# Optimization experiments

Measured on AMD Instinct MI355X. Metric: run time of the kernel, lower is better.

Reference implementation:

```python
import jax, jax.numpy as jnp
import numpy as np

B, S, N = 1, 256, 384
MSA_S, Z_D = 64, 128
H, C_H = 8, 32
C_OPM = 32
INF = 1e9

def ln(x, w, b):
    mu = jnp.mean(x, -1, keepdims=True)
    var = jnp.mean(jnp.square(x - mu), -1, keepdims=True)
    return (x - mu) * jax.lax.rsqrt(var + 1e-5) * w + b

def setup_inputs() -> dict:
    key = jax.random.key(0)
    ks = jax.random.split(key, 16)
    def lin(k, out_d, in_d):
        return jax.random.normal(k, (out_d, in_d), jnp.float32) / np.sqrt(in_d)
    return {
        "z": jax.random.normal(ks[0], (B, N, N, Z_D), jnp.float32),
        "m": jax.random.normal(ks[1], (B, S, N, MSA_S), jnp.float32),
        "token_mask": jnp.ones((B, N, N), jnp.float32),
        "msa_mask": jnp.ones((B, S, N), jnp.float32),
        "norm_z_w": jnp.ones((Z_D,), jnp.float32), "norm_z_b": jnp.zeros((Z_D,), jnp.float32),
        "proj_z_w": lin(ks[2], H, Z_D),
        "norm_m_w": jnp.ones((MSA_S,), jnp.float32), "norm_m_b": jnp.zeros((MSA_S,), jnp.float32),
        "proj_m_w": lin(ks[3], H * C_H, MSA_S),
        "proj_g_w": lin(ks[4], H * C_H, MSA_S),
        "pwa_proj_o_w": lin(ks[5], MSA_S, H * C_H),
        "trans_norm_w": jnp.ones((MSA_S,), jnp.float32), "trans_norm_b": jnp.zeros((MSA_S,), jnp.float32),
        "fc1_w": lin(ks[6], 4 * MSA_S, MSA_S),
        "fc2_w": lin(ks[7], 4 * MSA_S, MSA_S),
        "fc3_w": lin(ks[8], MSA_S, 4 * MSA_S),
        "opm_norm_w": jnp.ones((MSA_S,), jnp.float32), "opm_norm_b": jnp.zeros((MSA_S,), jnp.float32),
        "proj_a_w": lin(ks[9], C_OPM, MSA_S),
        "proj_b_w": lin(ks[10], C_OPM, MSA_S),
        "opm_proj_o_w": lin(ks[11], Z_D, C_OPM * C_OPM),
        "opm_proj_o_b": jnp.zeros((Z_D,), jnp.float32),
    }

def reference(z, m, token_mask, msa_mask,
              norm_z_w, norm_z_b, proj_z_w,
              norm_m_w, norm_m_b, proj_m_w, proj_g_w, pwa_proj_o_w,
              trans_norm_w, trans_norm_b, fc1_w, fc2_w, fc3_w,
              opm_norm_w, opm_norm_b, proj_a_w, proj_b_w, opm_proj_o_w, opm_proj_o_b):
    # --- PairWeightedAveraging: pair-biased, gated MSA row attention ---
    b_full = ln(z, norm_z_w, norm_z_b) @ proj_z_w.T                     # [B,N,N,H]
    bias = jnp.transpose(b_full, (0, 3, 1, 2)) + (1.0 - token_mask[:, None]) * (-INF)
    w = jax.nn.softmax(bias, axis=-1)                                   # [B,H,N,N]
    mn = ln(m, norm_m_w, norm_m_b)
    v = (mn @ proj_m_w.T).reshape(B, S, N, H, C_H)                      # [B,S,N,H,c]
    g = jax.nn.sigmoid(mn @ proj_g_w.T)                                 # [B,S,N,H*c]
    o = jnp.einsum('bhij,bsjhd->bsihd', w, v).reshape(B, S, N, H * C_H)
    m = m + (g * o) @ pwa_proj_o_w.T
    # --- MSA transition (SwiGLU) ---
    tn = ln(m, trans_norm_w, trans_norm_b)
    m = m + (jax.nn.silu(tn @ fc1_w.T) * (tn @ fc2_w.T)) @ fc3_w.T
    # --- OuterProductMean -> pair update ---
    mk = msa_mask[..., None]                                            # [B,S,N,1]
    on = ln(m, opm_norm_w, opm_norm_b)
    a = (on @ proj_a_w.T) * mk                                          # [B,S,N,c]
    bb = (on @ proj_b_w.T) * mk                                         # [B,S,N,c]
    num_mask = jnp.clip(jnp.einsum('bsi,bsj->bij', msa_mask, msa_mask), 1.0, None)[..., None]
    opm = jnp.einsum('bsic,bsjd->bijcd', a, bb).reshape(B, N, N, C_OPM * C_OPM) / num_mask
    z = z + opm @ opm_proj_o_w.T + opm_proj_o_b
    return (z, m)
```

## Files before the change

kernel.cpp:

```cpp
#include <hip/hip_runtime.h>
#include <math.h>

constexpr int NRES = 384;
constexpr int NSEQ = 256;
constexpr int DM   = 64;
constexpr int DZ   = 128;
constexpr int NH   = 8;
constexpr int DH   = 32;
constexpr int HC   = NH * DH;
constexpr int DOP  = 32;
constexpr int FF   = 4 * DM;

constexpr int NPAIR = NRES * NRES;
constexpr int NROWS = NSEQ * NRES;
constexpr int ZTOT  = NPAIR * DZ;
constexpr int SD    = NSEQ * DH;

typedef unsigned short ushort_t;
typedef unsigned char uchar_t;
typedef long long i64;
typedef __attribute__((ext_vector_type(8))) short short8;
typedef __attribute__((ext_vector_type(4))) float f32x4;
typedef __attribute__((ext_vector_type(4))) int int4_t;

__device__ __forceinline__ float wred_sum(float v) {
    #pragma unroll
    for (int off = 32; off; off >>= 1) v += __shfl_xor(v, off, 64);
    return v;
}
__device__ __forceinline__ float sigm(float x) { return 1.0f / (1.0f + expf(-x)); }
__device__ __forceinline__ ushort_t cvt_bf(float f) {
    unsigned u = __float_as_uint(f);
    unsigned r = (u + 0x7FFFu + ((u >> 16) & 1u)) >> 16;
    return (ushort_t)r;
}
__device__ __forceinline__ float cvt_f(ushort_t h) {
    return __uint_as_float(((unsigned)h) << 16);
}
__device__ __forceinline__ uchar_t cvt_f8(float f) {
    return (uchar_t)(__builtin_amdgcn_cvt_pk_fp8_f32(f, 0.0f, 0, 0) & 0xff);
}
__device__ __forceinline__ f32x4 mfma16(short8 a, short8 b, f32x4 c) {
    return __builtin_amdgcn_mfma_f32_16x16x32_bf16(a, b, c, 0, 0, 0);
}
__device__ __forceinline__ f32x4 mfma16f8(i64 a, i64 b, f32x4 c) {
    return __builtin_amdgcn_mfma_f32_16x16x32_fp8_fp8(a, b, c, 0, 0, 0);
}
__device__ __forceinline__ void gld16(const void* g, void* l) {
    __builtin_amdgcn_global_load_lds(
        (const __attribute__((address_space(1))) unsigned int*)g,
        (__attribute__((address_space(3))) unsigned int*)l, 16, 0, 0);
}

__global__ __launch_bounds__(256) void k_prep(const float* __restrict__ f1,
                                              const float* __restrict__ f2,
                                              const float* __restrict__ f3,
                                              const float* __restrict__ opW,
                                              const float* __restrict__ pmw,
                                              const float* __restrict__ pgw,
                                              const float* __restrict__ pow_,
                                              const float* __restrict__ paw,
                                              const float* __restrict__ pbw,
                                              const float* __restrict__ pzw,
                                              ushort_t* __restrict__ f1b,
                                              ushort_t* __restrict__ f2b,
                                              ushort_t* __restrict__ f3b,
                                              uchar_t* __restrict__ opW8,
                                              ushort_t* __restrict__ pmwb,
                                              ushort_t* __restrict__ pgwb,
                                              ushort_t* __restrict__ powb,
                                              ushort_t* __restrict__ abwb,
                                              ushort_t* __restrict__ pzwb) {
    int i = blockIdx.x * 256 + threadIdx.x;
    opW8[i] = cvt_f8(opW[i]);
    if (i < FF * DM) {
        f1b[i] = cvt_bf(f1[i]);
        f2b[i] = cvt_bf(f2[i]);
        f3b[i] = cvt_bf(f3[i]);
    }
    if (i < HC * DM) {
        pmwb[i] = cvt_bf(pmw[i]);
        pgwb[i] = cvt_bf(pgw[i]);
        powb[i] = cvt_bf(pow_[i]);
    }
    if (i < 2 * DOP * DM) {
        abwb[i] = cvt_bf(i < DOP * DM ? paw[i] : pbw[i - DOP * DM]);
    }
    if (i < 16 * DZ) {
        pzwb[i] = (i < NH * DZ) ? cvt_bf(pzw[i]) : (ushort_t)0;
    }
}

__global__ __launch_bounds__(256) void k_biassm(const float* __restrict__ z,
                                                const float* __restrict__ nzw,
                                                const float* __restrict__ nzb,
                                                const ushort_t* __restrict__ pzwb,
                                                const float* __restrict__ tmask,
                                                ushort_t* __restrict__ wsb) {
    int i = blockIdx.x;
    __shared__ ushort_t Azl[128][136];
    __shared__ ushort_t Bl[16][136];
    __shared__ float ob[8][388];
    __shared__ float wln[128], bln[128];
    int t = threadIdx.x;
    if (t < 128) { wln[t] = nzw[t]; bln[t] = nzb[t]; }
    int wave = t >> 6, lane = t & 63;
    int lk = (lane >> 4) * 8, lr = lane & 15;
    int wr = wave * 32;
    for (int idx = t * 8; idx < 16 * DZ; idx += 256 * 8) {
        int row = idx >> 7, col = idx & 127;
        *(short8*)&Bl[row][col] = *(const short8*)&pzwb[idx];
    }
    __syncthreads();
    for (int c = 0; c < 3; c++) {
        {
            int jl = t >> 1, cb = (t & 1) * 64;
            const float* src = &z[((size_t)i * NRES + c * 128 + jl) * DZ + cb];
            float4 v[16];
            float s1 = 0.0f, s2 = 0.0f;
            #pragma unroll
            for (int q = 0; q < 16; q++) {
                v[q] = *(const float4*)&src[q * 4];
                s1 += v[q].x + v[q].y + v[q].z + v[q].w;
                s2 += v[q].x * v[q].x + v[q].y * v[q].y + v[q].z * v[q].z + v[q].w * v[q].w;
            }
            s1 += __shfl_xor(s1, 1, 64);
            s2 += __shfl_xor(s2, 1, 64);
            float mu = s1 * (1.0f / 128.0f);
            float var = s2 * (1.0f / 128.0f) - mu * mu;
            float rs = rsqrtf(var + 1e-5f);
            #pragma unroll
            for (int q = 0; q < 8; q++) {
                float4 xa = v[2 * q], xb = v[2 * q + 1];
                int base = cb + q * 8;
                short8 o;
                o[0] = (short)cvt_bf((xa.x - mu) * rs * wln[base + 0] + bln[base + 0]);
                o[1] = (short)cvt_bf((xa.y - mu) * rs * wln[base + 1] + bln[base + 1]);
                o[2] = (short)cvt_bf((xa.z - mu) * rs * wln[base + 2] + bln[base + 2]);
                o[3] = (short)cvt_bf((xa.w - mu) * rs * wln[base + 3] + bln[base + 3]);
                o[4] = (short)cvt_bf((xb.x - mu) * rs * wln[base + 4] + bln[base + 4]);
                o[5] = (short)cvt_bf((xb.y - mu) * rs * wln[base + 5] + bln[base + 5]);
                o[6] = (short)cvt_bf((xb.z - mu) * rs * wln[base + 6] + bln[base + 6]);
                o[7] = (short)cvt_bf((xb.w - mu) * rs * wln[base + 7] + bln[base + 7]);
                *(short8*)&Azl[jl][base] = o;
            }
        }
        __syncthreads();
        f32x4 acc[2] = {};
        #pragma unroll
        for (int ks = 0; ks < 4; ks++) {
            short8 b = *(const short8*)&Bl[lr][ks * 32 + lk];
            short8 a0 = *(const short8*)&Azl[wr + lr][ks * 32 + lk];
            short8 a1 = *(const short8*)&Azl[wr + 16 + lr][ks * 32 + lk];
            acc[0] = mfma16(a0, b, acc[0]);
            acc[1] = mfma16(a1, b, acc[1]);
        }
        if (lr < NH) {
            #pragma unroll
            for (int ri = 0; ri < 2; ri++) {
                int jb = c * 128 + wr + 16 * ri + (lane >> 4) * 4;
                #pragma unroll
                for (int r = 0; r < 4; r++)
                    ob[lr][jb + r] = acc[ri][r];
            }
        }
        __syncthreads();
    }
    int h = wave * 2 + (lane >> 5);
    int l32 = lane & 31;
    int jb = l32 * 12;
    const float* tm = &tmask[(size_t)i * NRES];
    float vals[12];
    float mx = -1e30f;
    #pragma unroll
    for (int q = 0; q < 12; q++) {
        float v = ob[h][jb + q] + (1.0f - tm[jb + q]) * (-1e9f);
        vals[q] = v;
        mx = fmaxf(mx, v);
    }
    #pragma unroll
    for (int off = 16; off; off >>= 1) mx = fmaxf(mx, __shfl_xor(mx, off, 64));
    float sum = 0.0f;
    #pragma unroll
    for (int q = 0; q < 12; q++) { vals[q] = expf(vals[q] - mx); sum += vals[q]; }
    #pragma unroll
    for (int off = 16; off; off >>= 1) sum += __shfl_xor(sum, off, 64);
    float inv = 1.0f / sum;
    ushort_t* o = &wsb[(size_t)h * NPAIR + (size_t)i * NRES + jb];
    #pragma unroll
    for (int q = 0; q < 12; q++) o[q] = cvt_bf(vals[q] * inv);
}

__global__ __launch_bounds__(256) void k_ln64(const float* __restrict__ src,
                                              const float* __restrict__ lw,
                                              const float* __restrict__ lb,
                                              ushort_t* __restrict__ dst) {
    int wave = threadIdx.x >> 6, lane = threadIdx.x & 63;
    int r = blockIdx.x * 4 + wave;
    float x = src[(size_t)r * DM + lane];
    float mu = wred_sum(x) * (1.0f / 64.0f);
    float d = x - mu;
    float var = wred_sum(d * d) * (1.0f / 64.0f);
    dst[(size_t)r * DM + lane] = cvt_bf(d * rsqrtf(var + 1e-5f) * lw[lane] + lb[lane]);
}

__global__ __launch_bounds__(256) void k_vproj_mfma(const ushort_t* __restrict__ A,
                                                    const ushort_t* __restrict__ Bt,
                                                    ushort_t* __restrict__ vtt) {
    int m0 = blockIdx.y * 64, n0c = blockIdx.x * 64;
    __shared__ ushort_t Al[64][40];
    __shared__ ushort_t Bl[64][40];
    __shared__ ushort_t ot[64][72];
    int t = threadIdx.x;
    int srow = t >> 2, sko = (t & 3) * 8;
    int wave = t >> 6, lane = t & 63;
    int wr = (wave >> 1) * 32, wc = (wave & 1) * 32;
    int lk = (lane >> 4) * 8, lr = lane & 15;
    f32x4 acc[2][2] = {};
    for (int k0 = 0; k0 < DM; k0 += 32) {
        *(short8*)&Al[srow][sko] = *(const short8*)&A[(size_t)(m0 + srow) * DM + k0 + sko];
        *(short8*)&Bl[srow][sko] = *(const short8*)&Bt[(size_t)(n0c + srow) * DM + k0 + sko];
        __syncthreads();
        short8 a0 = *(const short8*)&Al[wr + lr][lk];
        short8 a1 = *(const short8*)&Al[wr + 16 + lr][lk];
        short8 b0 = *(const short8*)&Bl[wc + lr][lk];
        short8 b1 = *(const short8*)&Bl[wc + 16 + lr][lk];
        acc[0][0] = mfma16(a0, b0, acc[0][0]);
        acc[0][1] = mfma16(a0, b1, acc[0][1]);
        acc[1][0] = mfma16(a1, b0, acc[1][0]);
        acc[1][1] = mfma16(a1, b1, acc[1][1]);
        __syncthreads();
    }
    #pragma unroll
    for (int ri = 0; ri < 2; ri++)
        #pragma unroll
        for (int ci = 0; ci < 2; ci++) {
            int rowb = wr + 16 * ri + (lane >> 4) * 4;
            int colb = wc + 16 * ci + lr;
            #pragma unroll
            for (int r = 0; r < 4; r++)
                ot[colb][rowb + r] = cvt_bf(acc[ri][ci][r]);
        }
    __syncthreads();
    int s = m0 / NRES, n0 = m0 % NRES;
    int h0 = n0c >> 5;
    int orow = t >> 2, seg = (t & 3) * 16;
    short8 v0 = *(const short8*)&ot[orow][seg];
    short8 v1 = *(const short8*)&ot[orow][seg + 8];
    int hh = orow >> 5, dd = orow & 31;
    ushort_t* dst = &vtt[(((size_t)(h0 + hh) * SD) + s * DH + dd) * NRES + n0 + seg];
    *(short8*)&dst[0] = v0;
    *(short8*)&dst[8] = v1;
}

__global__ __launch_bounds__(256) void k_tr(const ushort_t* __restrict__ src,
                                            ushort_t* __restrict__ dst,
                                            int R, int C) {
    size_t bs = (size_t)R * C;
    const ushort_t* s = src + blockIdx.z * bs;
    ushort_t* d = dst + blockIdx.z * bs;
    int r0 = blockIdx.y * 64, c0 = blockIdx.x * 64;
    __shared__ ushort_t tile[64][72];
    int t = threadIdx.x;
    int tr = t >> 2, tc = (t & 3) * 16;
    *(short8*)&tile[tr][tc]     = *(const short8*)&s[(size_t)(r0 + tr) * C + c0 + tc];
    *(short8*)&tile[tr][tc + 8] = *(const short8*)&s[(size_t)(r0 + tr) * C + c0 + tc + 8];
    __syncthreads();
    short8 o0, o1;
    #pragma unroll
    for (int i = 0; i < 8; i++) {
        o0[i] = (short)tile[tc + i][tr];
        o1[i] = (short)tile[tc + 8 + i][tr];
    }
    *(short8*)&d[(size_t)(c0 + tr) * R + r0 + tc]     = o0;
    *(short8*)&d[(size_t)(c0 + tr) * R + r0 + tc + 8] = o1;
}

__global__ __launch_bounds__(256) void k_attn_mfma(const ushort_t* __restrict__ wsb,
                                                   const ushort_t* __restrict__ vtt,
                                                   ushort_t* __restrict__ otb2) {
    int h = blockIdx.z;
    const ushort_t* A  = wsb + (size_t)h * NPAIR;
    const ushort_t* Bt = vtt + (size_t)h * SD * NRES;
    int m0 = blockIdx.y * 128, n0 = blockIdx.x * 128;
    __shared__ ushort_t Al[128 * 32];
    __shared__ ushort_t Bl[128 * 32];
    int t = threadIdx.x;
    int w = t >> 6, lane = t & 63;
    int wr = (w >> 1) * 64, wc = (w & 1) * 64;
    int lq = lane >> 4, lr = lane & 15;
    int rS = w * 16 + (lane >> 2);
    int cqs = (((lane & 3) ^ ((rS >> 1) & 3)) << 3);
    f32x4 acc[4][4] = {};
    for (int k0 = 0; k0 < NRES; k0 += 32) {
        gld16(&A [(size_t)(m0 + rS)      * NRES + k0 + cqs], &Al[(w * 16) * 32]);
        gld16(&A [(size_t)(m0 + 64 + rS) * NRES + k0 + cqs], &Al[(64 + w * 16) * 32]);
        gld16(&Bt[(size_t)(n0 + rS)      * NRES + k0 + cqs], &Bl[(w * 16) * 32]);
        gld16(&Bt[(size_t)(n0 + 64 + rS) * NRES + k0 + cqs], &Bl[(64 + w * 16) * 32]);
        __syncthreads();
        short8 af[4], bf2[4];
        #pragma unroll
        for (int i = 0; i < 4; i++) {
            int ra = wr + 16 * i + lr;
            int rb = wc + 16 * i + lr;
            af[i]  = *(const short8*)&Al[ra * 32 + ((lq ^ ((ra >> 1) & 3)) << 3)];
            bf2[i] = *(const short8*)&Bl[rb * 32 + ((lq ^ ((rb >> 1) & 3)) << 3)];
        }
        #pragma unroll
        for (int ri = 0; ri < 4; ri++)
            #pragma unroll
            for (int ci = 0; ci < 4; ci++)
                acc[ri][ci] = mfma16(af[ri], bf2[ci], acc[ri][ci]);
        __syncthreads();
    }
    #pragma unroll
    for (int ri = 0; ri < 4; ri++)
        #pragma unroll
        for (int ci = 0; ci < 4; ci++) {
            int row0 = m0 + wr + 16 * ri + (lane >> 4) * 4;
            int col  = n0 + wc + 16 * ci + lr;
            int s = col >> 5, dd = col & 31;
            #pragma unroll
            for (int r = 0; r < 4; r++)
                otb2[((size_t)s * NRES + row0 + r) * HC + h * DH + dd] = cvt_bf(acc[ri][ci][r]);
        }
}

__global__ __launch_bounds__(256) void k_gateout(const ushort_t* __restrict__ A,
                                                 const ushort_t* __restrict__ Bg,
                                                 const ushort_t* __restrict__ otb2,
                                                 const ushort_t* __restrict__ Bo,
                                                 const float* __restrict__ m,
                                                 float* __restrict__ mout,
                                                 const float* __restrict__ tnw,
                                                 const float* __restrict__ tnb,
                                                 ushort_t* __restrict__ tn_bf) {
    int m0 = blockIdx.x * 64;
    __shared__ ushort_t Al[64][72];
    __shared__ ushort_t Bl[64][72];
    __shared__ ushort_t go[64][264];
    int t = threadIdx.x;
    int srow = t >> 2, sko = (t & 3) * 16;
    int wave = t >> 6, lane = t & 63;
    int wr = (wave >> 1) * 32, wc = (wave & 1) * 32;
    int lk = (lane >> 4) * 8, lr = lane & 15;
    float tw = tnw[lane], tb = tnb[lane];
    {
        const ushort_t* arow = &A[(size_t)(m0 + srow) * DM + sko];
        *(short8*)&Al[srow][sko]     = *(const short8*)&arow[0];
        *(short8*)&Al[srow][sko + 8] = *(const short8*)&arow[8];
    }
    __syncthreads();
    short8 a[2][2];
    a[0][0] = *(const short8*)&Al[wr + lr][lk];
    a[0][1] = *(const short8*)&Al[wr + lr][32 + lk];
    a[1][0] = *(const short8*)&Al[wr + 16 + lr][lk];
    a[1][1] = *(const short8*)&Al[wr + 16 + lr][32 + lk];
    for (int nq = 0; nq < 4; nq++) {
        __syncthreads();
        {
            const ushort_t* brow = &Bg[(size_t)(nq * 64 + srow) * DM + sko];
            *(short8*)&Bl[srow][sko]     = *(const short8*)&brow[0];
            *(short8*)&Bl[srow][sko + 8] = *(const short8*)&brow[8];
        }
        __syncthreads();
        f32x4 acc[2][2] = {};
        #pragma unroll
        for (int ks = 0; ks < 2; ks++) {
            short8 b0 = *(const short8*)&Bl[wc + lr][ks * 32 + lk];
            short8 b1 = *(const short8*)&Bl[wc + 16 + lr][ks * 32 + lk];
            acc[0][0] = mfma16(a[0][ks], b0, acc[0][0]);
            acc[0][1] = mfma16(a[0][ks], b1, acc[0][1]);
            acc[1][0] = mfma16(a[1][ks], b0, acc[1][0]);
            acc[1][1] = mfma16(a[1][ks], b1, acc[1][1]);
        }
        #pragma unroll
        for (int ri = 0; ri < 2; ri++)
            #pragma unroll
            for (int ci = 0; ci < 2; ci++) {
                int lrow = wr + 16 * ri + (lane >> 4) * 4;
                int col  = nq * 64 + wc + 16 * ci + lr;
                #pragma unroll
                for (int r = 0; r < 4; r++) {
                    float ov = cvt_f(otb2[(size_t)(m0 + lrow + r) * HC + col]);
                    go[lrow + r][col] = cvt_bf(sigm(acc[ri][ci][r]) * ov);
                }
            }
    }
    f32x4 acc[2][2] = {};
    for (int k0 = 0; k0 < HC; k0 += 32) {
        __syncthreads();
        *(short8*)&Bl[t >> 2][(t & 3) * 8] = *(const short8*)&Bo[(size_t)(t >> 2) * HC + k0 + (t & 3) * 8];
        __syncthreads();
        short8 a0 = *(const short8*)&go[wr + lr][k0 + lk];
        short8 a1 = *(const short8*)&go[wr + 16 + lr][k0 + lk];
        short8 b0 = *(const short8*)&Bl[wc + lr][lk];
        short8 b1 = *(const short8*)&Bl[wc + 16 + lr][lk];
        acc[0][0] = mfma16(a0, b0, acc[0][0]);
        acc[0][1] = mfma16(a0, b1, acc[0][1]);
        acc[1][0] = mfma16(a1, b0, acc[1][0]);
        acc[1][1] = mfma16(a1, b1, acc[1][1]);
    }
    __syncthreads();
    #pragma unroll
    for (int ri = 0; ri < 2; ri++)
        #pragma unroll
        for (int ci = 0; ci < 2; ci++) {
            int lrow0 = wr + 16 * ri + (lane >> 4) * 4;
            int col   = wc + 16 * ci + lr;
            #pragma unroll
            for (int r = 0; r < 4; r++) {
                size_t idx = (size_t)(m0 + lrow0 + r) * DM + col;
                float v = m[idx] + acc[ri][ci][r];
                mout[idx] = v;
                go[lrow0 + r][col] = cvt_bf(v);
            }
        }
    __syncthreads();
    for (int rr = 0; rr < 16; rr++) {
        int row = wave * 16 + rr;
        float x = cvt_f(go[row][lane]);
        float mu = wred_sum(x) * (1.0f / 64.0f);
        float d = x - mu;
        float var = wred_sum(d * d) * (1.0f / 64.0f);
        tn_bf[(size_t)(m0 + row) * DM + lane] = cvt_bf(d * rsqrtf(var + 1e-5f) * tw + tb);
    }
}

__global__ __launch_bounds__(256) void k_fctrans(const ushort_t* __restrict__ A,
                                                 const ushort_t* __restrict__ B1,
                                                 const ushort_t* __restrict__ B2,
                                                 const ushort_t* __restrict__ B3,
                                                 float* __restrict__ mio,
                                                 const float* __restrict__ onw,
                                                 const float* __restrict__ onb,
                                                 ushort_t* __restrict__ onb_bf) {
    int m0 = blockIdx.x * 64;
    __shared__ ushort_t Al[64][72];
    __shared__ ushort_t B1l[64][72];
    __shared__ ushort_t B2l[64][72];
    __shared__ ushort_t hhl[64][264];
    int t = threadIdx.x;
    int srow = t >> 2, sko = (t & 3) * 16;
    int wave = t >> 6, lane = t & 63;
    int wr = (wave >> 1) * 32, wc = (wave & 1) * 32;
    int lk = (lane >> 4) * 8, lr = lane & 15;
    float ow = onw[lane], ob = onb[lane];
    {
        const ushort_t* arow = &A[(size_t)(m0 + srow) * DM + sko];
        *(short8*)&Al[srow][sko]     = *(const short8*)&arow[0];
        *(short8*)&Al[srow][sko + 8] = *(const short8*)&arow[8];
    }
    __syncthreads();
    short8 a[2][2];
    a[0][0] = *(const short8*)&Al[wr + lr][lk];
    a[0][1] = *(const short8*)&Al[wr + lr][32 + lk];
    a[1][0] = *(const short8*)&Al[wr + 16 + lr][lk];
    a[1][1] = *(const short8*)&Al[wr + 16 + lr][32 + lk];
    for (int nq = 0; nq < 4; nq++) {
        __syncthreads();
        {
            const ushort_t* b1r = &B1[(size_t)(nq * 64 + srow) * DM + sko];
            const ushort_t* b2r = &B2[(size_t)(nq * 64 + srow) * DM + sko];
            *(short8*)&B1l[srow][sko]     = *(const short8*)&b1r[0];
            *(short8*)&B1l[srow][sko + 8] = *(const short8*)&b1r[8];
            *(short8*)&B2l[srow][sko]     = *(const short8*)&b2r[0];
            *(short8*)&B2l[srow][sko + 8] = *(const short8*)&b2r[8];
        }
        __syncthreads();
        f32x4 acc1[2][2] = {}, acc2[2][2] = {};
        #pragma unroll
        for (int ks = 0; ks < 2; ks++) {
            short8 p0 = *(const short8*)&B1l[wc + lr][ks * 32 + lk];
            short8 p1 = *(const short8*)&B1l[wc + 16 + lr][ks * 32 + lk];
            short8 q0 = *(const short8*)&B2l[wc + lr][ks * 32 + lk];
            short8 q1 = *(const short8*)&B2l[wc + 16 + lr][ks * 32 + lk];
            acc1[0][0] = mfma16(a[0][ks], p0, acc1[0][0]);
            acc1[0][1] = mfma16(a[0][ks], p1, acc1[0][1]);
            acc1[1][0] = mfma16(a[1][ks], p0, acc1[1][0]);
            acc1[1][1] = mfma16(a[1][ks], p1, acc1[1][1]);
            acc2[0][0] = mfma16(a[0][ks], q0, acc2[0][0]);
            acc2[0][1] = mfma16(a[0][ks], q1, acc2[0][1]);
            acc2[1][0] = mfma16(a[1][ks], q0, acc2[1][0]);
            acc2[1][1] = mfma16(a[1][ks], q1, acc2[1][1]);
        }
        #pragma unroll
        for (int ri = 0; ri < 2; ri++)
            #pragma unroll
            for (int ci = 0; ci < 2; ci++) {
                int lrow = wr + 16 * ri + (lane >> 4) * 4;
                int col  = nq * 64 + wc + 16 * ci + lr;
                #pragma unroll
                for (int r = 0; r < 4; r++) {
                    float a1v = acc1[ri][ci][r], a2v = acc2[ri][ci][r];
                    hhl[lrow + r][col] = cvt_bf(a1v * sigm(a1v) * a2v);
                }
            }
    }
    f32x4 acc[2][2] = {};
    for (int k0 = 0; k0 < FF; k0 += 32) {
        __syncthreads();
        *(short8*)&B1l[t >> 2][(t & 3) * 8] = *(const short8*)&B3[(size_t)(t >> 2) * FF + k0 + (t & 3) * 8];
        __syncthreads();
        short8 a0 = *(const short8*)&hhl[wr + lr][k0 + lk];
        short8 a1 = *(const short8*)&hhl[wr + 16 + lr][k0 + lk];
        short8 b0 = *(const short8*)&B1l[wc + lr][lk];
        short8 b1 = *(const short8*)&B1l[wc + 16 + lr][lk];
        acc[0][0] = mfma16(a0, b0, acc[0][0]);
        acc[0][1] = mfma16(a0, b1, acc[0][1]);
        acc[1][0] = mfma16(a1, b0, acc[1][0]);
        acc[1][1] = mfma16(a1, b1, acc[1][1]);
    }
    __syncthreads();
    #pragma unroll
    for (int ri = 0; ri < 2; ri++)
        #pragma unroll
        for (int ci = 0; ci < 2; ci++) {
            int lrow0 = wr + 16 * ri + (lane >> 4) * 4;
            int col   = wc + 16 * ci + lr;
            #pragma unroll
            for (int r = 0; r < 4; r++) {
                size_t idx = (size_t)(m0 + lrow0 + r) * DM + col;
                float v = mio[idx] + acc[ri][ci][r];
                mio[idx] = v;
                hhl[lrow0 + r][col] = cvt_bf(v);
            }
        }
    __syncthreads();
    for (int rr = 0; rr < 16; rr++) {
        int row = wave * 16 + rr;
        float x = cvt_f(hhl[row][lane]);
        float mu = wred_sum(x) * (1.0f / 64.0f);
        float d = x - mu;
        float var = wred_sum(d * d) * (1.0f / 64.0f);
        onb_bf[(size_t)(m0 + row) * DM + lane] = cvt_bf(d * rsqrtf(var + 1e-5f) * ow + ob);
    }
}

__global__ __launch_bounds__(256) void k_ab_mfma(const ushort_t* __restrict__ A,
                                                 const ushort_t* __restrict__ Bt,
                                                 const float* __restrict__ smask,
                                                 ushort_t* __restrict__ abuf,
                                                 ushort_t* __restrict__ bbuf) {
    int m0 = blockIdx.x * 64;
    __shared__ ushort_t Al[64][40];
    __shared__ ushort_t Bl[64][40];
    int t = threadIdx.x;
    int srow = t >> 2, sko = (t & 3) * 8;
    int wave = t >> 6, lane = t & 63;
    int wr = (wave >> 1) * 32, wc = (wave & 1) * 32;
    int lk = (lane >> 4) * 8, lr = lane & 15;
    f32x4 acc[2][2] = {};
    for (int k0 = 0; k0 < DM; k0 += 32) {
        *(short8*)&Al[srow][sko] = *(const short8*)&A[(size_t)(m0 + srow) * DM + k0 + sko];
        *(short8*)&Bl[srow][sko] = *(const short8*)&Bt[(size_t)srow * DM + k0 + sko];
        __syncthreads();
        short8 a0 = *(const short8*)&Al[wr + lr][lk];
        short8 a1 = *(const short8*)&Al[wr + 16 + lr][lk];
        short8 b0 = *(const short8*)&Bl[wc + lr][lk];
        short8 b1 = *(const short8*)&Bl[wc + 16 + lr][lk];
        acc[0][0] = mfma16(a0, b0, acc[0][0]);
        acc[0][1] = mfma16(a0, b1, acc[0][1]);
        acc[1][0] = mfma16(a1, b0, acc[1][0]);
        acc[1][1] = mfma16(a1, b1, acc[1][1]);
        __syncthreads();
    }
    #pragma unroll
    for (int ri = 0; ri < 2; ri++)
        #pragma unroll
        for (int ci = 0; ci < 2; ci++) {
            int row0 = m0 + wr + 16 * ri + (lane >> 4) * 4;
            int col  = wc + 16 * ci + lr;
            #pragma unroll
            for (int r = 0; r < 4; r++) {
                int rr = row0 + r;
                int s = rr / NRES, n = rr % NRES;
                float v = acc[ri][ci][r] * smask[rr];
                if (col < DOP)
                    abuf[(size_t)s * (NRES * DOP) + n * DOP + col] = cvt_bf(v);
                else
                    bbuf[(size_t)s * (NRES * DOP) + n * DOP + (col - DOP)] = cvt_bf(v);
            }
        }
}

__global__ __launch_bounds__(256) void k_msum(const float* __restrict__ smask,
                                              float* __restrict__ msum) {
    int i0 = blockIdx.y * 64, j0 = blockIdx.x * 64;
    __shared__ float As[16][64];
    __shared__ float Bs[16][64];
    int t = threadIdx.x;
    int ty = t >> 4, tx = t & 15;
    float acc[4][4] = {};
    for (int k0 = 0; k0 < NSEQ; k0 += 16) {
        int kk = t >> 4, x4 = (t & 15) * 4;
        *(float4*)&As[kk][x4] = *(const float4*)&smask[(size_t)(k0 + kk) * NRES + i0 + x4];
        *(float4*)&Bs[kk][x4] = *(const float4*)&smask[(size_t)(k0 + kk) * NRES + j0 + x4];
        __syncthreads();
        #pragma unroll
        for (int k = 0; k < 16; k++) {
            float4 a4 = *(const float4*)&As[k][ty * 4];
            float4 b4 = *(const float4*)&Bs[k][tx * 4];
            float ar[4] = {a4.x, a4.y, a4.z, a4.w};
            float br[4] = {b4.x, b4.y, b4.z, b4.w};
            #pragma unroll
            for (int i2 = 0; i2 < 4; i2++)
                #pragma unroll
                for (int j2 = 0; j2 < 4; j2++)
                    acc[i2][j2] += ar[i2] * br[j2];
        }
        __syncthreads();
    }
    #pragma unroll
    for (int r = 0; r < 4; r++) {
        float4 o4 = make_float4(fmaxf(acc[r][0], 1.0f), fmaxf(acc[r][1], 1.0f),
                                fmaxf(acc[r][2], 1.0f), fmaxf(acc[r][3], 1.0f));
        *(float4*)&msum[(size_t)(i0 + ty * 4 + r) * NRES + j0 + tx * 4] = o4;
    }
}

__global__ __launch_bounds__(256) void k_opm_mfma(const ushort_t* __restrict__ At,
                                                  const ushort_t* __restrict__ Bt,
                                                  uchar_t* __restrict__ opmc8) {
    int m0 = blockIdx.y * 128;
    int n0 = blockIdx.x * 128;
    __shared__ ushort_t Al[128 * 64];
    __shared__ ushort_t Bl[128 * 64];
    __shared__ uchar_t ol[16 * 1040];
    int t = threadIdx.x;
    int w = t >> 6, lane = t & 63;
    int wr = (w >> 1) * 64, wc = (w & 1) * 64;
    int lq = lane >> 4, lr = lane & 15;
    int rS = lane >> 3;
    int cqs = (((lane & 7) ^ rS) << 3);
    f32x4 acc[4][4] = {};
    for (int k0 = 0; k0 < NSEQ; k0 += 64) {
        #pragma unroll
        for (int g = 0; g < 4; g++) {
            int row = w * 32 + g * 8;
            gld16(&At[(size_t)(m0 + row + rS) * NSEQ + k0 + cqs], &Al[row * 64]);
            gld16(&Bt[(size_t)(n0 + row + rS) * NSEQ + k0 + cqs], &Bl[row * 64]);
        }
        __syncthreads();
        #pragma unroll
        for (int kk = 0; kk < 2; kk++) {
            short8 af[4], bf2[4];
            #pragma unroll
            for (int i = 0; i < 4; i++) {
                int ra = wr + 16 * i + lr;
                int rb = wc + 16 * i + lr;
                af[i]  = *(const short8*)&Al[ra * 64 + (((kk * 4 + lq) ^ (ra & 7)) << 3)];
                bf2[i] = *(const short8*)&Bl[rb * 64 + (((kk * 4 + lq) ^ (rb & 7)) << 3)];
            }
            #pragma unroll
            for (int ri = 0; ri < 4; ri++)
                #pragma unroll
                for (int ci = 0; ci < 4; ci++)
                    acc[ri][ci] = mfma16(bf2[ci], af[ri], acc[ri][ci]);
        }
        __syncthreads();
    }
    #pragma unroll
    for (int ri = 0; ri < 4; ri++)
        #pragma unroll
        for (int ci = 0; ci < 4; ci++) {
            int ml = wr + 16 * ri + lr;
            int il = ml >> 5, c = ml & 31;
            int nl = wc + 16 * ci + lq * 4;
            int j = nl >> 5, dd = nl & 31;
            int p = il * 4 + j;
            int p01  = __builtin_amdgcn_cvt_pk_fp8_f32(acc[ri][ci][0], acc[ri][ci][1], 0, 0);
            int pall = __builtin_amdgcn_cvt_pk_fp8_f32(acc[ri][ci][2], acc[ri][ci][3], p01, 1);
            *(int*)&ol[p * 1040 + (c << 5) + dd] = pall;
        }
    __syncthreads();
    {
        int p = t >> 4, off = (t & 15) * 64;
        int ilg = (m0 >> 5) + (p >> 2);
        int jg  = (n0 >> 5) + (p & 3);
        uchar_t* dst = &opmc8[((size_t)(ilg * NRES + jg) << 10) + off];
        const uchar_t* src = &ol[p * 1040 + off];
        #pragma unroll
        for (int q = 0; q < 4; q++)
            *(int4_t*)&dst[q * 16] = *(const int4_t*)&src[q * 16];
    }
}

__global__ __launch_bounds__(256) void k_proj_mfma(const uchar_t* __restrict__ A,
                                                   const uchar_t* __restrict__ Bt,
                                                   const float* __restrict__ opB,
                                                   const float* __restrict__ msum,
                                                   const float* __restrict__ zin,
                                                   float* __restrict__ zout,
                                                   int ib) {
    int m0 = blockIdx.x * 128;
    __shared__ uchar_t Al[128 * 32];
    __shared__ uchar_t Bl[128 * 32];
    int t = threadIdx.x;
    int w = t >> 6, lane = t & 63;
    int wr = (w >> 1) * 64, wc = (w & 1) * 64;
    int lq = lane >> 4, lr = lane & 15;
    int rS = lane >> 1, cS = (lane & 1) * 16;
    f32x4 acc[4][4] = {};
    for (int k0 = 0; k0 < 1024; k0 += 32) {
        gld16(&A [(size_t)(m0 + w * 32 + rS) * 1024 + k0 + cS], &Al[(w * 32) * 32]);
        gld16(&Bt[(size_t)(w * 32 + rS)      * 1024 + k0 + cS], &Bl[(w * 32) * 32]);
        __syncthreads();
        i64 af[4], bf2[4];
        #pragma unroll
        for (int i = 0; i < 4; i++) {
            af[i]  = *(const i64*)&Al[(wr + 16 * i + lr) * 32 + lq * 8];
            bf2[i] = *(const i64*)&Bl[(wc + 16 * i + lr) * 32 + lq * 8];
        }
        #pragma unroll
        for (int ri = 0; ri < 4; ri++)
            #pragma unroll
            for (int ci = 0; ci < 4; ci++)
                acc[ri][ci] = mfma16f8(bf2[ci], af[ri], acc[ri][ci]);
        __syncthreads();
    }
    #pragma unroll
    for (int ri = 0; ri < 4; ri++) {
        int p = m0 + wr + 16 * ri + lr;
        size_t G = (size_t)ib * NRES + p;
        float inv = 1.0f / msum[G];
        #pragma unroll
        for (int ci = 0; ci < 4; ci++) {
            int e0 = wc + 16 * ci + lq * 4;
            float4 zv = *(const float4*)&zin[G * DZ + e0];
            float4 bv = *(const float4*)&opB[e0];
            float4 o4;
            o4.x = zv.x + acc[ri][ci][0] * inv + bv.x;
            o4.y = zv.y + acc[ri][ci][1] * inv + bv.y;
            o4.z = zv.z + acc[ri][ci][2] * inv + bv.z;
            o4.w = zv.w + acc[ri][ci][3] * inv + bv.w;
            *(float4*)&zout[G * DZ + e0] = o4;
        }
    }
}

extern "C" void kernel_launch(void* const* d_in, const int* in_sizes, int n_in,
                              void* d_out, int out_size, void* d_ws, size_t ws_size,
                              hipStream_t stream) {
    const float* z     = (const float*)d_in[0];
    const float* m     = (const float*)d_in[1];
    const float* tmask = (const float*)d_in[2];
    const float* smask = (const float*)d_in[3];
    const float* nzw   = (const float*)d_in[4];
    const float* nzb   = (const float*)d_in[5];
    const float* pzw   = (const float*)d_in[6];
    const float* nmw   = (const float*)d_in[7];
    const float* nmb   = (const float*)d_in[8];
    const float* pmw   = (const float*)d_in[9];
    const float* pgw   = (const float*)d_in[10];
    const float* pow_  = (const float*)d_in[11];
    const float* tnw   = (const float*)d_in[12];
    const float* tnb_  = (const float*)d_in[13];
    const float* f1    = (const float*)d_in[14];
    const float* f2    = (const float*)d_in[15];
    const float* f3    = (const float*)d_in[16];
    const float* onw   = (const float*)d_in[17];
    const float* onb   = (const float*)d_in[18];
    const float* paw   = (const float*)d_in[19];
    const float* pbw   = (const float*)d_in[20];
    const float* opW   = (const float*)d_in[21];
    const float* opB   = (const float*)d_in[22];

    float* zout = (float*)d_out;
    float* mout = zout + ZTOT;

    char* W = (char*)d_ws;
    ushort_t* wsb  = (ushort_t*)(W + 4718592);
    ushort_t* mnb  = (ushort_t*)(W + 7077888);
    ushort_t* vtt  = (ushort_t*)(W + 69992448);
    ushort_t* otb2 = (ushort_t*)(W + 120324096);
    ushort_t* tn_bf  = vtt;
    ushort_t* onb_bf = mnb;
    ushort_t* abuf = (ushort_t*)(W + 69992448 + 12582912);
    ushort_t* bbuf = (ushort_t*)(W + 69992448 + 18874368);

    bool big = ws_size >= 348200000ull;
    int ichunk, nchunks;
    uchar_t *opmc8, *opW8;
    ushort_t *abt, *bbt;
    float* msum;
    ushort_t *f1b, *f2b, *f3b, *pmwb, *pgwb, *powb, *abwb, *pzwb;
    if (big) {
        ichunk = NRES; nchunks = 1;
        opmc8 = (uchar_t*)(W + 19660800);
        abt  = (ushort_t*)(W + 321650688);
        bbt  = (ushort_t*)(W + 327942144);
        msum = (float*)(W + 346816512);
        f1b  = (ushort_t*)(W + 347406336);
        f2b  = (ushort_t*)(W + 347439104);
        f3b  = (ushort_t*)(W + 347471872);
        opW8 = (uchar_t*)(W + 347504640);
        pmwb = (ushort_t*)(W + 347766784);
        pgwb = (ushort_t*)(W + 347799552);
        powb = (ushort_t*)(W + 347832320);
        abwb = (ushort_t*)(W + 347865088);
        pzwb = (ushort_t*)(W + 347873280);
    } else {
        ichunk = 96; nchunks = 4;
        opmc8 = (uchar_t*)(W + 19660800);
        abt  = otb2;
        bbt  = (ushort_t*)(W + 120324096 + 6291456);
        msum = (float*)(W + 170655744);
        f1b  = (ushort_t*)(W + 171245568);
        f2b  = (ushort_t*)(W + 171278336);
        f3b  = (ushort_t*)(W + 171311104);
        opW8 = (uchar_t*)(W + 171343872);
        pmwb = (ushort_t*)(W + 171606016);
        pgwb = (ushort_t*)(W + 171638784);
        powb = (ushort_t*)(W + 171671552);
        abwb = (ushort_t*)(W + 171704320);
        pzwb = (ushort_t*)(W + 171712512);
    }

    k_prep<<<512, 256, 0, stream>>>(f1, f2, f3, opW, pmw, pgw, pow_, paw, pbw, pzw,
                                    f1b, f2b, f3b, opW8, pmwb, pgwb, powb, abwb, pzwb);

    k_biassm<<<NRES, 256, 0, stream>>>(z, nzw, nzb, pzwb, tmask, wsb);
    k_ln64<<<NROWS / 4, 256, 0, stream>>>(m, nmw, nmb, mnb);
    k_vproj_mfma<<<dim3(HC / 64, NROWS / 64), 256, 0, stream>>>(mnb, pmwb, vtt);
    k_attn_mfma<<<dim3(SD / 128, NRES / 128, NH), 256, 0, stream>>>(wsb, vtt, otb2);
    k_gateout<<<NROWS / 64, 256, 0, stream>>>(mnb, pgwb, otb2, powb, m, mout, tnw, tnb_, tn_bf);

    k_fctrans<<<NROWS / 64, 256, 0, stream>>>(tn_bf, f1b, f2b, f3b, mout, onw, onb, onb_bf);

    k_ab_mfma<<<NROWS / 64, 256, 0, stream>>>(onb_bf, abwb, smask, abuf, bbuf);
    k_tr<<<dim3((NRES * DOP) / 64, NSEQ / 64, 2), 256, 0, stream>>>(abuf, abt, NSEQ, NRES * DOP);
    k_msum<<<dim3(NRES / 64, NRES / 64), 256, 0, stream>>>(smask, msum);
    for (int cb = 0; cb < nchunks; cb++) {
        int ib = cb * ichunk;
        const ushort_t* Achunk = abt + (size_t)(ib * DOP) * NSEQ;
        k_opm_mfma<<<dim3((NRES * DOP) / 128, (ichunk * DOP) / 128), 256, 0, stream>>>(Achunk, bbt, opmc8);
        k_proj_mfma<<<(ichunk * NRES) / 128, 256, 0, stream>>>(opmc8, opW8, opB, msum, z, zout, ib);
    }
}
```

Measured before the change: 454.4 us.

## Fuse OPM output projection into outer-product kernel, dropping fp8 intermediate

The outer-product kernel now projects its 16 pair tiles (each 32x32 fp8) through the 1024x128 output weight itself, using fp8 MFMA with weights staged through LDS, and writes the final z update directly. This removes the separate projection kernel and the global round trip of the large fp8 opm intermediate. In exchange, every block re-reads the full projection weight and the projection runs with only 16 rows per MFMA tile in each block, so efficiency is lower. LDS is reused between the A/B staging and the output tile.

```diff
diff --git a/kernel.cpp b/kernel.cpp
--- a/kernel.cpp
+++ b/kernel.cpp
@@ -621,18 +621,26 @@
 
 __global__ __launch_bounds__(256) void k_opm_mfma(const ushort_t* __restrict__ At,
                                                   const ushort_t* __restrict__ Bt,
-                                                  uchar_t* __restrict__ opmc8) {
+                                                  const uchar_t* __restrict__ opW8,
+                                                  const float* __restrict__ opB,
+                                                  const float* __restrict__ msum,
+                                                  const float* __restrict__ zin,
+                                                  float* __restrict__ zout,
+                                                  int ib) {
     int m0 = blockIdx.y * 128;
     int n0 = blockIdx.x * 128;
-    __shared__ ushort_t Al[128 * 64];
-    __shared__ ushort_t Bl[128 * 64];
-    __shared__ uchar_t ol[16 * 1040];
+    __shared__ ushort_t ABl[2 * 128 * 64];
+    __shared__ uchar_t Wl[128 * 128];
+    ushort_t* Al = ABl;
+    ushort_t* Bl = ABl + 128 * 64;
+    uchar_t* ol = (uchar_t*)ABl;
     int t = threadIdx.x;
     int w = t >> 6, lane = t & 63;
     int wr = (w >> 1) * 64, wc = (w & 1) * 64;
     int lq = lane >> 4, lr = lane & 15;
     int rS = lane >> 3;
     int cqs = (((lane & 7) ^ rS) << 3);
+    int cS8 = (((lane & 7) ^ rS) << 4);
     f32x4 acc[4][4] = {};
     for (int k0 = 0; k0 < NSEQ; k0 += 64) {
         #pragma unroll
@@ -674,66 +682,44 @@
             *(int*)&ol[p * 1040 + (c << 5) + dd] = pall;
         }
     __syncthreads();
+    f32x4 accp[2] = {};
+    for (int kc = 0; kc < 8; kc++) {
+        #pragma unroll
+        for (int g = 0; g < 4; g++) {
+            int row = w * 32 + g * 8;
+            gld16(&opW8[(size_t)(row + rS) * 1024 + kc * 128 + cS8], &Wl[row * 128]);
+        }
+        __syncthreads();
+        #pragma unroll
+        for (int ls = 0; ls < 4; ls++) {
+            i64 af = *(const i64*)&ol[lr * 1040 + kc * 128 + ls * 32 + lq * 8];
+            int l = ls * 2 + (lq >> 1);
+            int wo = (lq & 1) * 8;
+            #pragma unroll
+            for (int et = 0; et < 2; et++) {
+                int er = w * 32 + et * 16 + lr;
+                i64 bf = *(const i64*)&Wl[er * 128 + ((l ^ (er & 7)) << 4) + wo];
+                accp[et] = mfma16f8(bf, af, accp[et]);
+            }
+        }
+        __syncthreads();
+    }
     {
-        int p = t >> 4, off = (t & 15) * 64;
-        int ilg = (m0 >> 5) + (p >> 2);
+        int p = lr;
+        int ilg = ib + (m0 >> 5) + (p >> 2);
         int jg  = (n0 >> 5) + (p & 3);
-        uchar_t* dst = &opmc8[((size_t)(ilg * NRES + jg) << 10) + off];
-        const uchar_t* src = &ol[p * 1040 + off];
-        #pragma unroll
-        for (int q = 0; q < 4; q++)
-            *(int4_t*)&dst[q * 16] = *(const int4_t*)&src[q * 16];
-    }
-}
-
-__global__ __launch_bounds__(256) void k_proj_mfma(const uchar_t* __restrict__ A,
-                                                   const uchar_t* __restrict__ Bt,
-                                                   const float* __restrict__ opB,
-                                                   const float* __restrict__ msum,
-                                                   const float* __restrict__ zin,
-                                                   float* __restrict__ zout,
-                                                   int ib) {
-    int m0 = blockIdx.x * 128;
-    __shared__ uchar_t Al[128 * 32];
-    __shared__ uchar_t Bl[128 * 32];
-    int t = threadIdx.x;
-    int w = t >> 6, lane = t & 63;
-    int wr = (w >> 1) * 64, wc = (w & 1) * 64;
-    int lq = lane >> 4, lr = lane & 15;
-    int rS = lane >> 1, cS = (lane & 1) * 16;
-    f32x4 acc[4][4] = {};
-    for (int k0 = 0; k0 < 1024; k0 += 32) {
-        gld16(&A [(size_t)(m0 + w * 32 + rS) * 1024 + k0 + cS], &Al[(w * 32) * 32]);
-        gld16(&Bt[(size_t)(w * 32 + rS)      * 1024 + k0 + cS], &Bl[(w * 32) * 32]);
-        __syncthreads();
-        i64 af[4], bf2[4];
-        #pragma unroll
-        for (int i = 0; i < 4; i++) {
-            af[i]  = *(const i64*)&Al[(wr + 16 * i + lr) * 32 + lq * 8];
-            bf2[i] = *(const i64*)&Bl[(wc + 16 * i + lr) * 32 + lq * 8];
-        }
-        #pragma unroll
-        for (int ri = 0; ri < 4; ri++)
-            #pragma unroll
-            for (int ci = 0; ci < 4; ci++)
-                acc[ri][ci] = mfma16f8(bf2[ci], af[ri], acc[ri][ci]);
-        __syncthreads();
-    }
-    #pragma unroll
-    for (int ri = 0; ri < 4; ri++) {
-        int p = m0 + wr + 16 * ri + lr;
-        size_t G = (size_t)ib * NRES + p;
+        size_t G = (size_t)ilg * NRES + jg;
         float inv = 1.0f / msum[G];
         #pragma unroll
-        for (int ci = 0; ci < 4; ci++) {
-            int e0 = wc + 16 * ci + lq * 4;
+        for (int et = 0; et < 2; et++) {
+            int e0 = w * 32 + et * 16 + lq * 4;
             float4 zv = *(const float4*)&zin[G * DZ + e0];
             float4 bv = *(const float4*)&opB[e0];
             float4 o4;
-            o4.x = zv.x + acc[ri][ci][0] * inv + bv.x;
-            o4.y = zv.y + acc[ri][ci][1] * inv + bv.y;
-            o4.z = zv.z + acc[ri][ci][2] * inv + bv.z;
-            o4.w = zv.w + acc[ri][ci][3] * inv + bv.w;
+            o4.x = zv.x + accp[et][0] * inv + bv.x;
+            o4.y = zv.y + accp[et][1] * inv + bv.y;
+            o4.z = zv.z + accp[et][2] * inv + bv.z;
+            o4.w = zv.w + accp[et][3] * inv + bv.w;
             *(float4*)&zout[G * DZ + e0] = o4;
         }
     }
@@ -781,13 +767,12 @@
 
     bool big = ws_size >= 348200000ull;
     int ichunk, nchunks;
-    uchar_t *opmc8, *opW8;
+    uchar_t *opW8;
     ushort_t *abt, *bbt;
     float* msum;
     ushort_t *f1b, *f2b, *f3b, *pmwb, *pgwb, *powb, *abwb, *pzwb;
     if (big) {
         ichunk = NRES; nchunks = 1;
-        opmc8 = (uchar_t*)(W + 19660800);
         abt  = (ushort_t*)(W + 321650688);
         bbt  = (ushort_t*)(W + 327942144);
         msum = (float*)(W + 346816512);
@@ -802,7 +787,6 @@
         pzwb = (ushort_t*)(W + 347873280);
     } else {
         ichunk = 96; nchunks = 4;
-        opmc8 = (uchar_t*)(W + 19660800);
         abt  = otb2;
         bbt  = (ushort_t*)(W + 120324096 + 6291456);
         msum = (float*)(W + 170655744);
@@ -834,7 +818,7 @@
     for (int cb = 0; cb < nchunks; cb++) {
         int ib = cb * ichunk;
         const ushort_t* Achunk = abt + (size_t)(ib * DOP) * NSEQ;
-        k_opm_mfma<<<dim3((NRES * DOP) / 128, (ichunk * DOP) / 128), 256, 0, stream>>>(Achunk, bbt, opmc8);
-        k_proj_mfma<<<(ichunk * NRES) / 128, 256, 0, stream>>>(opmc8, opW8, opB, msum, z, zout, ib);
-    }
-}
+        k_opm_mfma<<<dim3((NRES * DOP) / 128, (ichunk * DOP) / 128), 256, 0, stream>>>(
+            Achunk, bbt, opW8, opB, msum, z, zout, ib);
+    }
+}
```

New measurement: 413.2 us. 9.1% less time.
